# Kernel optimization log

Hardware: AMD Instinct MI355X
Metric: run time of the kernel (lower is better)

## Reference

```python
import jax, jax.numpy as jnp
import numpy as np

DECAY = 0.85          # decay_factor
LAM = 0.5             # lambda_diversity
EPS = 1e-12


def setup_inputs() -> dict:
    key = jax.random.key(0)
    ks = jax.random.split(key, 6)
    N, D = 32768, 512
    return {
        "predictions": jax.random.normal(ks[0], (N,), jnp.float32),
        "target_scores": jax.random.normal(ks[1], (N,), jnp.float32),
        "context_embeddings": jax.random.normal(ks[2], (N, D), jnp.float32),
        "input_embeddings": jax.random.normal(ks[3], (N, D), jnp.float32),
        "dsm_embeddings": jax.random.normal(ks[4], (N, D), jnp.float32),
        "explanation_embeddings": jax.random.normal(ks[5], (N, D), jnp.float32),
        "k": 16,
    }


def reference(predictions, target_scores, context_embeddings, input_embeddings,
              dsm_embeddings, explanation_embeddings, k):
    # relevance probabilities over all N candidates (dim=0 softmax as in torch)
    rel = jax.nn.softmax(predictions.squeeze(), axis=0)

    # L2-normalize once so cos_sim is a plain dot product
    E = explanation_embeddings
    En = E / (jnp.linalg.norm(E, axis=-1, keepdims=True) + EPS)  # [N, D]
    N = En.shape[0]

    # Greedy ERR/MMR relevance-diversity selection of k items:
    #   score_t(i) = decay^t * rel[i] - lambda * max_{j in selected} cos(E_i, E_j)
    # pick argmax over unselected; err_score_t = decay^t * rel[selected_t]
    def step(carry, t):
        mask, max_sim = carry                       # [N] bool, [N] f32
        decay = DECAY ** t.astype(rel.dtype)
        score = decay * rel - LAM * max_sim
        score = jnp.where(mask, -jnp.inf, score)
        idx = jnp.argmax(score)
        err = rel[idx] * decay
        sim_new = En @ En[idx]                      # cos sim of all to new pick
        return (mask.at[idx].set(True),
                jnp.maximum(max_sim, sim_new)), (err, idx)

    init = (jnp.zeros((N,), bool), jnp.zeros((N,), rel.dtype))
    _, (errs, sel) = jax.lax.scan(step, init, jnp.arange(k))

    err_loss = -jnp.sum(errs)

    # mmr_loss = -sum_i max_j cos(E_i, E_j) over selected set (self included,
    # exactly as the original code does with util.cos_sim(...).max())
    S = En[sel]                                    # [k, D]
    sims = S @ S.T                                 # [k, k]
    mmr_loss = -jnp.sum(jnp.max(sims, axis=1))

    return err_loss + LAM * mmr_loss
```

## Files before the change

kernel.cpp:

```cpp
#include <hip/hip_runtime.h>
#include <cmath>


#define DECAYF 0.85f
#define LAMF   0.5f
#define EPSF   1e-12f

constexpr int D    = 512;
constexpr int KMAX = 16;
constexpr int NBLK = 256;
constexpr int TPB  = 1024;
constexpr int RPW  = 8;
constexpr int RPB  = 128;

using u32 = unsigned int;
using u64 = unsigned long long;

__device__ inline float wsum(float v) {
#pragma unroll
    for (int o = 32; o > 0; o >>= 1) v += __shfl_xor(v, o);
    return v;
}
__device__ inline float wmaxf(float v) {
#pragma unroll
    for (int o = 32; o > 0; o >>= 1) v = fmaxf(v, __shfl_xor(v, o));
    return v;
}
__device__ inline u64 wmax64(u64 v) {
#pragma unroll
    for (int o = 32; o > 0; o >>= 1) {
        u64 w = __shfl_xor(v, o);
        v = (w > v) ? w : v;
    }
    return v;
}
__device__ inline u32 fkey(float f) {
    u32 u = __float_as_uint(f);
    return (u & 0x80000000u) ? ~u : (u | 0x80000000u);
}
__device__ inline u64 poll_slot(u64* p) {
    u64 v = __hip_atomic_load(p, __ATOMIC_RELAXED, __HIP_MEMORY_SCOPE_AGENT);
    while (v == 0ull) {
        __builtin_amdgcn_s_sleep(1);
        v = __hip_atomic_load(p, __ATOMIC_RELAXED, __HIP_MEMORY_SCOPE_AGENT);
    }
    return v;
}
__device__ inline void publish(u64* p, u64 v) {
    __hip_atomic_store(p, v, __ATOMIC_RELAXED, __HIP_MEMORY_SCOPE_AGENT);
}

__global__ __launch_bounds__(TPB, 4) void fused_kernel(
        const float* __restrict__ pred,
        const float* __restrict__ E,
        const int*   __restrict__ kptr,
        float* __restrict__ out,
        u64*   __restrict__ sm,
        u64*   __restrict__ part,
        u64*   __restrict__ bcast) {
    const int b = blockIdx.x, tid = threadIdx.x;
    const int wv = tid >> 6, lane = tid & 63;

    __shared__ float pred_s[RPB];
    __shared__ float rel_s[RPB];
    __shared__ float msim_s[RPB];
    __shared__ u64   bkey_s[RPB];
    __shared__ u64   scan_s[NBLK];
    __shared__ float m_s, S_s;
    __shared__ int   j_s;
    __shared__ int   sel_s[KMAX];
    __shared__ float invsel_s[KMAX];
    __shared__ float rmax_s[KMAX];

    int kk = kptr[0];
    if (kk > KMAX) kk = KMAX;
    if (kk < 0) kk = 0;

    if (tid < RPB) pred_s[tid] = pred[b * RPB + tid];
    __syncthreads();
    if (wv == 0) {
        float p0 = pred_s[lane], p1 = pred_s[lane + 64];
        float mb = wmaxf(fmaxf(p0, p1));
        float sb = wsum(expf(p0 - mb) + expf(p1 - mb));
        if (lane == 0)
            publish(&sm[b], ((u64)__float_as_uint(mb) << 32) | __float_as_uint(sb));
    }
    asm volatile("" ::: "memory");

    const int row0 = b * RPB + wv * RPW;
    float r[RPW][8];
#pragma unroll
    for (int rr = 0; rr < RPW; ++rr) {
        const float4* p = (const float4*)(E + (size_t)(row0 + rr) * D) + 2 * lane;
        float4 a0 = p[0], a1 = p[1];
        r[rr][0] = a0.x; r[rr][1] = a0.y; r[rr][2] = a0.z; r[rr][3] = a0.w;
        r[rr][4] = a1.x; r[rr][5] = a1.y; r[rr][6] = a1.z; r[rr][7] = a1.w;
        float ss = 0.f;
#pragma unroll
        for (int e = 0; e < 8; ++e) ss += r[rr][e] * r[rr][e];
        ss = wsum(ss);
        float inv = 1.f / (sqrtf(ss) + EPSF);
#pragma unroll
        for (int e = 0; e < 8; ++e) r[rr][e] *= inv;
        asm volatile("" : "+v"(r[rr][0]), "+v"(r[rr][1]), "+v"(r[rr][2]), "+v"(r[rr][3]),
                          "+v"(r[rr][4]), "+v"(r[rr][5]), "+v"(r[rr][6]), "+v"(r[rr][7]));
    }

    if (tid < NBLK) scan_s[tid] = poll_slot(&sm[tid]);
    __syncthreads();
    if (wv == 0) {
        u64 v0 = scan_s[lane], v1 = scan_s[lane + 64],
            v2 = scan_s[lane + 128], v3 = scan_s[lane + 192];
        float m0 = __uint_as_float((u32)(v0 >> 32)), m1 = __uint_as_float((u32)(v1 >> 32));
        float m2 = __uint_as_float((u32)(v2 >> 32)), m3 = __uint_as_float((u32)(v3 >> 32));
        float M = wmaxf(fmaxf(fmaxf(m0, m1), fmaxf(m2, m3)));
        float acc = __uint_as_float((u32)(v0 & 0xFFFFFFFFull)) * expf(m0 - M)
                  + __uint_as_float((u32)(v1 & 0xFFFFFFFFull)) * expf(m1 - M)
                  + __uint_as_float((u32)(v2 & 0xFFFFFFFFull)) * expf(m2 - M)
                  + __uint_as_float((u32)(v3 & 0xFFFFFFFFull)) * expf(m3 - M);
        acc = wsum(acc);
        if (lane == 0) { m_s = M; S_s = acc; }
    }
    __syncthreads();
    const float M    = m_s;
    const float Sinv = 1.f / S_s;
    if (tid < RPB) { rel_s[tid] = expf(pred_s[tid] - M) * Sinv; msim_s[tid] = 0.f; }
    __syncthreads();

    for (int t = 0; t < KMAX; ++t) {
        if (t >= kk) break;
        const float decay = powf(DECAYF, (float)t);
        if (tid < RPB) {
            const float sc = decay * rel_s[tid] - LAMF * msim_s[tid];
            bkey_s[tid] = ((u64)fkey(sc) << 32) | (u32)~(u32)(b * RPB + tid);
        }
        __syncthreads();
        if (wv == 0) {
            u64 v = bkey_s[lane], w = bkey_s[lane + 64];
            v = (w > v) ? w : v;
            v = wmax64(v);
            if (lane == 0) publish(&part[t * NBLK + b], v);
        }
        if (b == 0) {
            if (tid < NBLK) scan_s[tid] = poll_slot(&part[t * NBLK + tid]);
            __syncthreads();
            if (wv == 0) {
                u64 v = scan_s[lane];
                u64 w = scan_s[lane + 64];  v = (w > v) ? w : v;
                w = scan_s[lane + 128];     v = (w > v) ? w : v;
                w = scan_s[lane + 192];     v = (w > v) ? w : v;
                v = wmax64(v);
                if (lane == 0) publish(&bcast[t], v);
            }
        }
        if (tid == 0)
            j_s = (int)~(u32)(poll_slot(&bcast[t]) & 0xFFFFFFFFull);
        __syncthreads();
        const int j = j_s;
        if (tid == 0) {
            sel_s[t] = j;
            if (j >= b * RPB && j < (b + 1) * RPB)
                msim_s[j - b * RPB] = INFINITY;
        }
        __syncthreads();
        if (t < kk - 1) {
            const float4* pj = (const float4*)(E + (size_t)j * D) + 2 * lane;
            float4 b0 = pj[0], b1 = pj[1];
            float bj[8] = {b0.x, b0.y, b0.z, b0.w, b1.x, b1.y, b1.z, b1.w};
            float ss = 0.f;
#pragma unroll
            for (int e = 0; e < 8; ++e) ss += bj[e] * bj[e];
            ss = wsum(ss);
            const float js = 1.f / (sqrtf(ss) + EPSF);
#pragma unroll
            for (int e = 0; e < 8; ++e) bj[e] *= js;
#pragma unroll
            for (int rr = 0; rr < RPW; ++rr) {
                float d = 0.f;
#pragma unroll
                for (int e = 0; e < 8; ++e) d += r[rr][e] * bj[e];
                d = wsum(d);
                if (lane == 0) {
                    const int lr = wv * RPW + rr;
                    msim_s[lr] = fmaxf(msim_s[lr], d);
                }
            }
            __syncthreads();
        }
    }

    if (b == 0) {
        if (wv < kk) {
            const int si = sel_s[wv];
            const float4* pa = (const float4*)(E + (size_t)si * D) + 2 * lane;
            float4 a0 = pa[0], a1 = pa[1];
            float ss = a0.x*a0.x + a0.y*a0.y + a0.z*a0.z + a0.w*a0.w
                     + a1.x*a1.x + a1.y*a1.y + a1.z*a1.z + a1.w*a1.w;
            ss = wsum(ss);
            if (lane == 0) invsel_s[wv] = 1.f / (sqrtf(ss) + EPSF);
        }
        __syncthreads();
        if (wv < kk) {
            const int si = sel_s[wv];
            const float4* pa = (const float4*)(E + (size_t)si * D) + 2 * lane;
            float4 a0 = pa[0], a1 = pa[1];
            const float ia = invsel_s[wv];
            float av[8] = {a0.x * ia, a0.y * ia, a0.z * ia, a0.w * ia,
                           a1.x * ia, a1.y * ia, a1.z * ia, a1.w * ia};
            float m = -INFINITY;
            for (int jj = 0; jj < kk; ++jj) {
                const float4* pb = (const float4*)(E + (size_t)sel_s[jj] * D) + 2 * lane;
                float4 c0 = pb[0], c1 = pb[1];
                float d = av[0]*c0.x + av[1]*c0.y + av[2]*c0.z + av[3]*c0.w
                        + av[4]*c1.x + av[5]*c1.y + av[6]*c1.z + av[7]*c1.w;
                d = wsum(d);
                m = fmaxf(m, d * invsel_s[jj]);
            }
            if (lane == 0) rmax_s[wv] = m;
        }
        __syncthreads();
        if (tid == 0) {
            float es = 0.f, mm = 0.f;
            for (int t = 0; t < kk; ++t) {
                es += powf(DECAYF, (float)t) * expf(pred[sel_s[t]] - M) * Sinv;
                mm += rmax_s[t];
            }
            out[0] = -es - LAMF * mm;
        }
    }
}

extern "C" void kernel_launch(void* const* d_in, const int* in_sizes, int n_in,
                              void* d_out, int out_size, void* d_ws, size_t ws_size,
                              hipStream_t stream) {
    const float* pred = (const float*)d_in[0];
    const float* E    = (const float*)d_in[5];
    const int*   kptr = (const int*)d_in[6];
    float* out        = (float*)d_out;

    u64* sm    = (u64*)d_ws;
    u64* part  = sm + NBLK;
    u64* bcast = part + KMAX * NBLK;
    hipMemsetAsync(d_ws, 0, (NBLK + KMAX * NBLK + KMAX) * sizeof(u64), stream);

    void* args[] = {(void*)&pred, (void*)&E, (void*)&kptr, (void*)&out,
                    (void*)&sm, (void*)&part, (void*)&bcast};
    hipLaunchCooperativeKernel((const void*)fused_kernel,
                               dim3(NBLK), dim3(TPB), args, 0, stream);
}
```

Measured before the change: 137.6 us.

## Keep per-row scores in registers and fold sim update into next step

Halves threads per block to 512 with 16 rows per wave, holding rel and max-sim in registers instead of shared memory. The similarity update for the previous pick moves to the start of the next iteration, which removes several block barriers per step. A per-wave argmax key now replaces the per-row key array. The spin-wait sleep is dropped so polling reacts sooner, at the cost of more memory traffic while waiting, and register pressure rises because each thread now keeps 16 rows of embedding data.

```diff
diff --git a/kernel.cpp b/kernel.cpp
--- a/kernel.cpp
+++ b/kernel.cpp
@@ -9,9 +9,10 @@
 constexpr int D    = 512;
 constexpr int KMAX = 16;
 constexpr int NBLK = 256;
-constexpr int TPB  = 1024;
-constexpr int RPW  = 8;
-constexpr int RPB  = 128;
+constexpr int TPB  = 512;
+constexpr int NW   = TPB / 64;
+constexpr int RPW  = 16;
+constexpr int RPB  = NW * RPW;
 
 using u32 = unsigned int;
 using u64 = unsigned long long;
@@ -40,17 +41,15 @@
 }
 __device__ inline u64 poll_slot(u64* p) {
     u64 v = __hip_atomic_load(p, __ATOMIC_RELAXED, __HIP_MEMORY_SCOPE_AGENT);
-    while (v == 0ull) {
-        __builtin_amdgcn_s_sleep(1);
+    while (v == 0ull)
         v = __hip_atomic_load(p, __ATOMIC_RELAXED, __HIP_MEMORY_SCOPE_AGENT);
-    }
     return v;
 }
 __device__ inline void publish(u64* p, u64 v) {
     __hip_atomic_store(p, v, __ATOMIC_RELAXED, __HIP_MEMORY_SCOPE_AGENT);
 }
 
-__global__ __launch_bounds__(TPB, 4) void fused_kernel(
+__global__ __launch_bounds__(TPB, 2) void fused_kernel(
         const float* __restrict__ pred,
         const float* __restrict__ E,
         const int*   __restrict__ kptr,
@@ -62,9 +61,7 @@
     const int wv = tid >> 6, lane = tid & 63;
 
     __shared__ float pred_s[RPB];
-    __shared__ float rel_s[RPB];
-    __shared__ float msim_s[RPB];
-    __shared__ u64   bkey_s[RPB];
+    __shared__ u64   wkey_s[NW];
     __shared__ u64   scan_s[NBLK];
     __shared__ float m_s, S_s;
     __shared__ int   j_s;
@@ -124,20 +121,50 @@
     __syncthreads();
     const float M    = m_s;
     const float Sinv = 1.f / S_s;
-    if (tid < RPB) { rel_s[tid] = expf(pred_s[tid] - M) * Sinv; msim_s[tid] = 0.f; }
-    __syncthreads();
-
+
+    float rel_r[RPW], msim_r[RPW];
+#pragma unroll
+    for (int rr = 0; rr < RPW; ++rr) {
+        rel_r[rr]  = expf(pred_s[wv * RPW + rr] - M) * Sinv;
+        msim_r[rr] = 0.f;
+    }
+
+    int jprev = -1;
     for (int t = 0; t < KMAX; ++t) {
         if (t >= kk) break;
         const float decay = powf(DECAYF, (float)t);
-        if (tid < RPB) {
-            const float sc = decay * rel_s[tid] - LAMF * msim_s[tid];
-            bkey_s[tid] = ((u64)fkey(sc) << 32) | (u32)~(u32)(b * RPB + tid);
-        }
+        if (t > 0) {
+            const float4* pj = (const float4*)(E + (size_t)jprev * D) + 2 * lane;
+            float4 b0 = pj[0], b1 = pj[1];
+            float bj[8] = {b0.x, b0.y, b0.z, b0.w, b1.x, b1.y, b1.z, b1.w};
+            float ss = 0.f;
+#pragma unroll
+            for (int e = 0; e < 8; ++e) ss += bj[e] * bj[e];
+            ss = wsum(ss);
+            const float js = 1.f / (sqrtf(ss) + EPSF);
+#pragma unroll
+            for (int e = 0; e < 8; ++e) bj[e] *= js;
+#pragma unroll
+            for (int rr = 0; rr < RPW; ++rr) {
+                float d = 0.f;
+#pragma unroll
+                for (int e = 0; e < 8; ++e) d += r[rr][e] * bj[e];
+                d = wsum(d);
+                msim_r[rr] = (row0 + rr == jprev) ? INFINITY
+                                                  : fmaxf(msim_r[rr], d);
+            }
+        }
+        u64 best = 0ull;
+#pragma unroll
+        for (int rr = 0; rr < RPW; ++rr) {
+            const float sc = decay * rel_r[rr] - LAMF * msim_r[rr];
+            const u64 key = ((u64)fkey(sc) << 32) | (u32)~(u32)(row0 + rr);
+            best = (key > best) ? key : best;
+        }
+        if (lane == 0) wkey_s[wv] = best;
         __syncthreads();
         if (wv == 0) {
-            u64 v = bkey_s[lane], w = bkey_s[lane + 64];
-            v = (w > v) ? w : v;
+            u64 v = (lane < NW) ? wkey_s[lane] : 0ull;
             v = wmax64(v);
             if (lane == 0) publish(&part[t * NBLK + b], v);
         }
@@ -153,58 +180,31 @@
                 if (lane == 0) publish(&bcast[t], v);
             }
         }
-        if (tid == 0)
-            j_s = (int)~(u32)(poll_slot(&bcast[t]) & 0xFFFFFFFFull);
-        __syncthreads();
-        const int j = j_s;
         if (tid == 0) {
+            const int j = (int)~(u32)(poll_slot(&bcast[t]) & 0xFFFFFFFFull);
+            j_s = j;
             sel_s[t] = j;
-            if (j >= b * RPB && j < (b + 1) * RPB)
-                msim_s[j - b * RPB] = INFINITY;
-        }
-        __syncthreads();
-        if (t < kk - 1) {
-            const float4* pj = (const float4*)(E + (size_t)j * D) + 2 * lane;
-            float4 b0 = pj[0], b1 = pj[1];
-            float bj[8] = {b0.x, b0.y, b0.z, b0.w, b1.x, b1.y, b1.z, b1.w};
-            float ss = 0.f;
-#pragma unroll
-            for (int e = 0; e < 8; ++e) ss += bj[e] * bj[e];
-            ss = wsum(ss);
-            const float js = 1.f / (sqrtf(ss) + EPSF);
-#pragma unroll
-            for (int e = 0; e < 8; ++e) bj[e] *= js;
-#pragma unroll
-            for (int rr = 0; rr < RPW; ++rr) {
-                float d = 0.f;
-#pragma unroll
-                for (int e = 0; e < 8; ++e) d += r[rr][e] * bj[e];
-                d = wsum(d);
-                if (lane == 0) {
-                    const int lr = wv * RPW + rr;
-                    msim_s[lr] = fmaxf(msim_s[lr], d);
-                }
-            }
-            __syncthreads();
-        }
+        }
+        __syncthreads();
+        jprev = j_s;
     }
 
     if (b == 0) {
-        if (wv < kk) {
-            const int si = sel_s[wv];
+        for (int ii = wv; ii < kk; ii += NW) {
+            const int si = sel_s[ii];
             const float4* pa = (const float4*)(E + (size_t)si * D) + 2 * lane;
             float4 a0 = pa[0], a1 = pa[1];
             float ss = a0.x*a0.x + a0.y*a0.y + a0.z*a0.z + a0.w*a0.w
                      + a1.x*a1.x + a1.y*a1.y + a1.z*a1.z + a1.w*a1.w;
             ss = wsum(ss);
-            if (lane == 0) invsel_s[wv] = 1.f / (sqrtf(ss) + EPSF);
-        }
-        __syncthreads();
-        if (wv < kk) {
-            const int si = sel_s[wv];
+            if (lane == 0) invsel_s[ii] = 1.f / (sqrtf(ss) + EPSF);
+        }
+        __syncthreads();
+        for (int ii = wv; ii < kk; ii += NW) {
+            const int si = sel_s[ii];
             const float4* pa = (const float4*)(E + (size_t)si * D) + 2 * lane;
             float4 a0 = pa[0], a1 = pa[1];
-            const float ia = invsel_s[wv];
+            const float ia = invsel_s[ii];
             float av[8] = {a0.x * ia, a0.y * ia, a0.z * ia, a0.w * ia,
                            a1.x * ia, a1.y * ia, a1.z * ia, a1.w * ia};
             float m = -INFINITY;
@@ -216,7 +216,7 @@
                 d = wsum(d);
                 m = fmaxf(m, d * invsel_s[jj]);
             }
-            if (lane == 0) rmax_s[wv] = m;
+            if (lane == 0) rmax_s[ii] = m;
         }
         __syncthreads();
         if (tid == 0) {
```

Measured after the change: 156.8 us. +13.9%, slower.
